# Performance work log

Hardware: AMD Instinct MI355X
Metric: run time of the kernel (lower is better)

The kernel has to match this reference:

```python
import jax, jax.numpy as jnp
import numpy as np

SPECIES = [1, 6, 7, 8]
N_SPECIES = len(SPECIES)
MAX_Z = max(SPECIES) + 1  # 9
N_IN = 256
N_HIDDEN = 512
N_OUT = 1
N_ATOMS = 65536


def setup_inputs() -> dict:
    key = jax.random.key(0)
    ks = jax.random.split(key, 9)
    x = jax.random.normal(ks[0], (N_ATOMS, N_IN), dtype=jnp.float32)
    z = jax.random.randint(ks[1], (N_ATOMS,), 0, MAX_Z)
    s = 0.05
    # Stacked per-species MLP parameters: [S, ...]
    W1 = jax.random.normal(ks[2], (N_SPECIES, N_HIDDEN, N_IN), dtype=jnp.float32) * s
    b1 = jax.random.normal(ks[3], (N_SPECIES, N_HIDDEN), dtype=jnp.float32) * s
    W2 = jax.random.normal(ks[4], (N_SPECIES, N_HIDDEN, N_HIDDEN), dtype=jnp.float32) * s
    b2 = jax.random.normal(ks[5], (N_SPECIES, N_HIDDEN), dtype=jnp.float32) * s
    W3 = jax.random.normal(ks[6], (N_SPECIES, N_OUT, N_HIDDEN), dtype=jnp.float32) * s
    b3 = jax.random.normal(ks[7], (N_SPECIES, N_OUT), dtype=jnp.float32) * s
    # One-hot embedding table [MAX_Z, N_SPECIES]: row Z has 1.0 at its species slot
    E = np.zeros((MAX_Z, N_SPECIES), dtype=np.float32)
    for idx, Z in enumerate(SPECIES):
        E[Z, idx] = 1.0
    E = jnp.asarray(E)
    return {"x": x, "z": z, "W1": W1, "b1": b1, "W2": W2, "b2": b2,
            "W3": W3, "b3": b3, "E": E}


def reference(x, z, W1, b1, W2, b2, W3, b3, E):
    # Every atom runs through all species MLPs (dense, O(N*S)), as in the original.
    # h1: [N, S, H]
    h1 = jnp.tanh(jnp.einsum('ni,shi->nsh', x, W1) + b1[None])
    h2 = jnp.tanh(jnp.einsum('nsh,sgh->nsg', h1, W2) + b2[None])
    # out_s: [N, S, n_out] -> [N, S*n_out] (n_out == 1 -> [N, S])
    out_s = (jnp.einsum('nsh,soh->nso', h2, W3) + b3[None]).reshape(x.shape[0], -1)
    gate = E[z]  # [N, S] embedding lookup (one-hot hard routing)
    return jnp.sum(out_s * gate, axis=1)  # [N]
```

## Files before the change

kernel.cpp:

```cpp
#include <hip/hip_runtime.h>

typedef __attribute__((ext_vector_type(8))) short bf16x8;
typedef __attribute__((ext_vector_type(4))) float f32x4;
typedef __attribute__((ext_vector_type(2))) unsigned int u32x2;
typedef unsigned short us;

#define NATOMS 65536
#define NIN 256
#define NHID 512
#define TM 128
#define LDB 528

__device__ __forceinline__ us f2b(float f) {
    union { float f; unsigned int u; } a; a.f = f;
    unsigned int r = a.u + 0x7FFFu + ((a.u >> 16) & 1u);
    return (us)(r >> 16);
}
__device__ __forceinline__ float fast_tanh(float v) {
    float t = __builtin_amdgcn_exp2f(v * 2.88539008f);
    float r = __builtin_amdgcn_rcpf(t + 1.f);
    return __builtin_fmaf(-2.f, r, 1.f);
}
__device__ __forceinline__ unsigned cvt_pk(float lo, float hi) {
    unsigned p;
    asm("v_cvt_pk_bf16_f32 %0, %1, %2" : "=v"(p) : "v"(lo), "v"(hi));
    return p;
}

__global__ __launch_bounds__(1024) void setup_kernel(
    const float* __restrict__ W1, const float* __restrict__ W2,
    const float* __restrict__ W3,
    us* __restrict__ W1p, us* __restrict__ W2p, us* __restrict__ W3b,
    const int* __restrict__ z, int* __restrict__ cnt,
    int* __restrict__ lists, float* __restrict__ out) {
    int tid = threadIdx.x;
    int blk = blockIdx.x;
    if (blk < 64) {
        __shared__ int lcnt[4];
        __shared__ int gbase[4];
        __shared__ int wbase[16][4];
        int wv = tid >> 6;
        int lane = tid & 63;
        if (tid < 4) lcnt[tid] = 0;
        __syncthreads();

        int i = blk * 1024 + tid;
        int zz = z[i];
        int s = (zz == 1) ? 0 : (zz == 6) ? 1 : (zz == 7) ? 2 : (zz == 8) ? 3 : -1;
        if (s < 0) out[i] = 0.f;

        int prefix = 0;
#pragma unroll
        for (int sp = 0; sp < 4; ++sp) {
            unsigned long long m = __ballot(s == sp);
            if (m) {
                int c = __popcll(m);
                int leader = __ffsll((long long)m) - 1;
                if (lane == leader) wbase[wv][sp] = atomicAdd(&lcnt[sp], c);
                if (s == sp) prefix = __popcll(m & ((1ull << lane) - 1ull));
            }
        }
        __syncthreads();
        if (tid < 4) gbase[tid] = atomicAdd(&cnt[tid], lcnt[tid]);
        __syncthreads();
        if (s >= 0) lists[s * NATOMS + gbase[s] + wbase[wv][s] + prefix] = i;
    } else {
        int i = (blk - 64) * 1024 + tid;
        if (i < 65536) {
            int s = i >> 14;
            int n = (i >> 5) & 511;
            int k8 = i & 31;
            const float* src = W1 + (size_t)i * 8;
            us p[8];
#pragma unroll
            for (int j = 0; j < 8; ++j) p[j] = f2b(src[j]);
            int ntile = n >> 4, nl = n & 15;
            int kstep = k8 >> 2, kq = k8 & 3;
            int lane = kq * 16 + nl;
            size_t chunk = ((size_t)(s * 32 + ntile) * 8 + kstep) * 64 + lane;
            *(uint4*)(W1p + chunk * 8) = *(uint4*)p;
        }
        if (i < 131072) {
            int s = i >> 15;
            int n = (i >> 6) & 511;
            int k8 = i & 63;
            const float* src = W2 + (size_t)i * 8;
            us p[8];
#pragma unroll
            for (int j = 0; j < 8; ++j) p[j] = f2b(src[j]);
            int ntile = n >> 4, nl = n & 15;
            int kstep = k8 >> 2, kq = k8 & 3;
            int lane = kq * 16 + nl;
            size_t chunk = ((size_t)(s * 32 + ntile) * 16 + kstep) * 64 + lane;
            *(uint4*)(W2p + chunk * 8) = *(uint4*)p;
        }
        if (i < 2048) W3b[i] = f2b(W3[i]);
    }
}

template<int K>
__device__ __forceinline__ void gemm8(const char* ldsLo, const char* ldsHi, const us* Wp,
                                      int lane, int wtile, f32x4 acc[8][4]) {
    constexpr int KS = K / 32;
    const us* wp[4];
#pragma unroll
    for (int nt = 0; nt < 4; ++nt)
        wp[nt] = Wp + (((size_t)(wtile + nt) * KS) * 64 + lane) * 8;
    int aoff[8];
#pragma unroll
    for (int mt = 0; mt < 8; ++mt)
        aoff[mt] = (mt * 16 + (lane & 15)) * LDB + (((lane >> 4) << 3) << 1);

    bf16x8 a0[4], a1[4], b[2][4];
#pragma unroll
    for (int nt = 0; nt < 4; ++nt) b[0][nt] = *(const bf16x8*)wp[nt];
#pragma unroll
    for (int mt = 0; mt < 4; ++mt) a0[mt] = *(const bf16x8*)(ldsLo + aoff[mt]);

#pragma unroll
    for (int i = 0; i < KS; ++i) {
        const int bc = i & 1;
        const char* srcI = (i < 8) ? (ldsLo + i * 64) : (ldsHi + (i - 8) * 64);
#pragma unroll
        for (int mt = 0; mt < 4; ++mt)
            a1[mt] = *(const bf16x8*)(srcI + aoff[4 + mt]);
        if (i + 1 < KS) {
#pragma unroll
            for (int nt = 0; nt < 4; ++nt)
                b[bc ^ 1][nt] = *(const bf16x8*)(wp[nt] + (i + 1) * 512);
        }
        __builtin_amdgcn_s_setprio(1);
#pragma unroll
        for (int nt = 0; nt < 4; ++nt)
#pragma unroll
            for (int mt = 0; mt < 4; ++mt)
                acc[mt][nt] = __builtin_amdgcn_mfma_f32_16x16x32_bf16(a0[mt], b[bc][nt], acc[mt][nt], 0, 0, 0);
        __builtin_amdgcn_s_setprio(0);
        if (i + 1 < KS) {
            const char* srcN = (i + 1 < 8) ? (ldsLo + (i + 1) * 64) : (ldsHi + (i + 1 - 8) * 64);
#pragma unroll
            for (int mt = 0; mt < 4; ++mt)
                a0[mt] = *(const bf16x8*)(srcN + aoff[mt]);
        }
        __builtin_amdgcn_s_setprio(1);
#pragma unroll
        for (int nt = 0; nt < 4; ++nt)
#pragma unroll
            for (int mt = 0; mt < 4; ++mt)
                acc[4 + mt][nt] = __builtin_amdgcn_mfma_f32_16x16x32_bf16(a1[mt], b[bc][nt], acc[4 + mt][nt], 0, 0, 0);
        __builtin_amdgcn_s_setprio(0);
    }
}

__device__ __forceinline__ void act_store_split(char* bufA, char* bufB,
                                                const float* __restrict__ bias,
                                                int lane, int ncb, f32x4 acc[8][4]) {
    char* dstBase = (ncb < 256) ? bufA : bufB;
    int coff = (ncb < 256) ? ncb : (ncb - 256);
#pragma unroll
    for (int nt = 0; nt < 4; ++nt) {
        int nl = coff + nt * 16 + (lane & 15);
        float bv = bias[ncb + nt * 16 + (lane & 15)];
#pragma unroll
        for (int mt = 0; mt < 8; ++mt) {
            float t0 = fast_tanh(acc[mt][nt][0] + bv);
            float t1 = fast_tanh(acc[mt][nt][1] + bv);
            float t2 = fast_tanh(acc[mt][nt][2] + bv);
            float t3 = fast_tanh(acc[mt][nt][3] + bv);
            unsigned p01 = cvt_pk(t0, t1);
            unsigned p23 = cvt_pk(t2, t3);
            int row0 = mt * 16 + ((lane >> 4) << 2);
            char* base = dstBase + row0 * LDB + nl * 2;
            *(us*)(base)           = (us)p01;
            *(us*)(base + LDB)     = (us)(p01 >> 16);
            *(us*)(base + 2 * LDB) = (us)p23;
            *(us*)(base + 3 * LDB) = (us)(p23 >> 16);
        }
    }
}

__global__ __launch_bounds__(512, 1) void mlp_kernel(
    const float* __restrict__ x, const int* __restrict__ cnt, const int* __restrict__ lists,
    const us* __restrict__ W1p, const us* __restrict__ W2p, const us* __restrict__ W3b,
    const float* __restrict__ b1, const float* __restrict__ b2, const float* __restrict__ b3,
    float* __restrict__ out) {
    int bx = blockIdx.x;
    int s = bx & 3;
    int t = bx >> 2;
    int base = t * TM;
    int n_s = cnt[s];
    if (base >= n_s) return;
    const int* list = lists + s * NATOMS;
    int cnt_t = n_s - base; if (cnt_t > TM) cnt_t = TM;

    __shared__ __align__(16) char bufA[TM * LDB];
    __shared__ __align__(16) char bufB[TM * LDB];

    int tid = threadIdx.x;
    int lane = tid & 63;
    int w = tid >> 6;
    int wtile = w * 4;
    int ncb = w * 64;

    {
        int r = tid >> 2;
        int cb = (tid & 3) * 64;
        int atom = (r < cnt_t) ? list[base + r] : -1;
        const float* xr = x + (size_t)(atom < 0 ? 0 : atom) * NIN;
#pragma unroll
        for (int j = 0; j < 16; ++j) {
            int c = cb + j * 4;
            float4 v;
            if (atom >= 0) v = *(const float4*)(xr + c);
            else v = make_float4(0.f, 0.f, 0.f, 0.f);
            u32x2 p;
            p.x = cvt_pk(v.x, v.y);
            p.y = cvt_pk(v.z, v.w);
            *(u32x2*)(bufB + r * LDB + c * 2) = p;
        }
    }
    __syncthreads();

    {
        f32x4 acc[8][4];
#pragma unroll
        for (int i = 0; i < 8; ++i)
#pragma unroll
            for (int j = 0; j < 4; ++j) acc[i][j] = (f32x4){0.f, 0.f, 0.f, 0.f};
        gemm8<NIN>(bufB, bufB, W1p + (size_t)s * NHID * NIN, lane, wtile, acc);
        __syncthreads();
        act_store_split(bufA, bufB, b1 + s * NHID, lane, ncb, acc);
    }
    __syncthreads();

    {
        f32x4 acc[8][4];
#pragma unroll
        for (int i = 0; i < 8; ++i)
#pragma unroll
            for (int j = 0; j < 4; ++j) acc[i][j] = (f32x4){0.f, 0.f, 0.f, 0.f};
        gemm8<NHID>(bufA, bufB, W2p + (size_t)s * NHID * NHID, lane, wtile, acc);
        __syncthreads();
        act_store_split(bufA, bufB, b2 + s * NHID, lane, ncb, acc);
    }
    __syncthreads();

    {
        int m = tid >> 2;
        int q = tid & 3;
        const us* W3s = W3b + (size_t)s * NHID;
        const char* src = (q < 2) ? bufA : bufB;
        int cbase = (q < 2) ? q * 128 : q * 128 - 256;
        float sum = 0.f;
#pragma unroll
        for (int j = 0; j < 16; ++j) {
            int hh = cbase + j * 8;
            bf16x8 hv = *(const bf16x8*)(src + m * LDB + hh * 2);
            bf16x8 wv = *(const bf16x8*)(W3s + q * 128 + j * 8);
#pragma unroll
            for (int e = 0; e < 8; ++e) {
                union { unsigned u; float f; } ha, wa;
                ha.u = ((unsigned)(us)hv[e]) << 16;
                wa.u = ((unsigned)(us)wv[e]) << 16;
                sum += ha.f * wa.f;
            }
        }
        sum += __shfl_xor(sum, 1);
        sum += __shfl_xor(sum, 2);
        if (q == 0 && m < cnt_t) out[list[base + m]] = sum + b3[s];
    }
}

extern "C" void kernel_launch(void* const* d_in, const int* in_sizes, int n_in,
                              void* d_out, int out_size, void* d_ws, size_t ws_size,
                              hipStream_t stream) {
    const float* x  = (const float*)d_in[0];
    const int*   z  = (const int*)d_in[1];
    const float* W1 = (const float*)d_in[2];
    const float* b1 = (const float*)d_in[3];
    const float* W2 = (const float*)d_in[4];
    const float* b2 = (const float*)d_in[5];
    const float* W3 = (const float*)d_in[6];
    const float* b3 = (const float*)d_in[7];
    float* out = (float*)d_out;

    char* ws = (char*)d_ws;
    int* cnt = (int*)ws;
    int* lists = (int*)(ws + 256);
    us* W1p = (us*)(ws + 256 + (size_t)4 * NATOMS * 4);
    us* W2p = W1p + 4 * NHID * NIN;
    us* W3b = W2p + 4 * NHID * NHID;

    (void)hipMemsetAsync(cnt, 0, 16, stream);
    setup_kernel<<<192, 1024, 0, stream>>>(W1, W2, W3, W1p, W2p, W3b, z, cnt, lists, out);
    mlp_kernel<<<256, 512, 0, stream>>>(x, cnt, lists, W1p, W2p, W3b, b1, b2, b3, out);
}
```

Baseline: 55.29 us.

## Split fused MLP into layer1 and layer2+3 kernels with smaller tiles

Replaces the single fused 128-row MLP kernel with two kernels: layer 1 writes bf16 hidden activations to a workspace buffer, then layer 2+3 reads them back in 32-row tiles. The smaller tiles give more blocks (512 and 1024 instead of 256) to fill the GPU's compute units and shrink per-block LDS. The cost is an extra launch plus a global round trip of the h1 activations. The fused path is kept as a fallback when the workspace is too small, and the per-species MAXROWS cap of 8192 assumes each species gets at most that many atoms.

```diff
diff --git a/kernel.cpp b/kernel.cpp
--- a/kernel.cpp
+++ b/kernel.cpp
@@ -10,6 +10,9 @@
 #define NHID 512
 #define TM 128
 #define LDB 528
+#define MAXROWS 8192
+#define LDBX 528
+#define LDBH 1040
 
 __device__ __forceinline__ us f2b(float f) {
     union { float f; unsigned int u; } a; a.f = f;
@@ -271,6 +274,231 @@
     }
 }
 
+__global__ __launch_bounds__(512, 1) void layer1_kernel(
+    const float* __restrict__ x, const int* __restrict__ cnt, const int* __restrict__ lists,
+    const us* __restrict__ W1p, const float* __restrict__ b1, us* __restrict__ h1buf) {
+    int bx = blockIdx.x;
+    int s = bx & 3;
+    int t = bx >> 2;
+    int base = t * 64;
+    int n_s = cnt[s];
+    if (base >= n_s) return;
+    const int* list = lists + s * NATOMS;
+    int cnt_t = n_s - base; if (cnt_t > 64) cnt_t = 64;
+
+    __shared__ __align__(16) char bufX[64 * LDBX];
+
+    int tid = threadIdx.x;
+    int lane = tid & 63;
+    int w = tid >> 6;
+    int wtile = w * 4;
+    int ncb = w * 64;
+
+    {
+        int r = tid >> 3;
+        int cb = (tid & 7) * 32;
+        int atom = (r < cnt_t) ? list[base + r] : -1;
+        const float* xr = x + (size_t)(atom < 0 ? 0 : atom) * NIN;
+#pragma unroll
+        for (int j = 0; j < 8; ++j) {
+            int c = cb + j * 4;
+            float4 v;
+            if (atom >= 0) v = *(const float4*)(xr + c);
+            else v = make_float4(0.f, 0.f, 0.f, 0.f);
+            u32x2 p;
+            p.x = cvt_pk(v.x, v.y);
+            p.y = cvt_pk(v.z, v.w);
+            *(u32x2*)(bufX + r * LDBX + c * 2) = p;
+        }
+    }
+    __syncthreads();
+
+    f32x4 acc[4][4];
+#pragma unroll
+    for (int i = 0; i < 4; ++i)
+#pragma unroll
+        for (int j = 0; j < 4; ++j) acc[i][j] = (f32x4){0.f, 0.f, 0.f, 0.f};
+    {
+        const us* Wp = W1p + (size_t)s * NHID * NIN;
+        const us* wp[4];
+#pragma unroll
+        for (int nt = 0; nt < 4; ++nt)
+            wp[nt] = Wp + (((size_t)(wtile + nt) * 8) * 64 + lane) * 8;
+        int aoff[4];
+#pragma unroll
+        for (int mt = 0; mt < 4; ++mt)
+            aoff[mt] = (mt * 16 + (lane & 15)) * LDBX + (((lane >> 4) << 3) << 1);
+
+        bf16x8 b[2][4];
+#pragma unroll
+        for (int nt = 0; nt < 4; ++nt) b[0][nt] = *(const bf16x8*)wp[nt];
+#pragma unroll
+        for (int i = 0; i < 8; ++i) {
+            const int bc = i & 1;
+            if (i + 1 < 8) {
+#pragma unroll
+                for (int nt = 0; nt < 4; ++nt)
+                    b[bc ^ 1][nt] = *(const bf16x8*)(wp[nt] + (i + 1) * 512);
+            }
+            bf16x8 a[4];
+#pragma unroll
+            for (int mt = 0; mt < 4; ++mt)
+                a[mt] = *(const bf16x8*)(bufX + aoff[mt] + i * 64);
+            __builtin_amdgcn_s_setprio(1);
+#pragma unroll
+            for (int nt = 0; nt < 4; ++nt)
+#pragma unroll
+                for (int mt = 0; mt < 4; ++mt)
+                    acc[mt][nt] = __builtin_amdgcn_mfma_f32_16x16x32_bf16(b[bc][nt], a[mt], acc[mt][nt], 0, 0, 0);
+            __builtin_amdgcn_s_setprio(0);
+        }
+    }
+
+    us* h1seg = h1buf + (size_t)s * MAXROWS * NHID;
+#pragma unroll
+    for (int nt = 0; nt < 4; ++nt) {
+        int n0 = ncb + nt * 16 + ((lane >> 4) << 2);
+        float4 bv = *(const float4*)(b1 + s * NHID + n0);
+#pragma unroll
+        for (int mt = 0; mt < 4; ++mt) {
+            int m = mt * 16 + (lane & 15);
+            float t0 = fast_tanh(acc[mt][nt][0] + bv.x);
+            float t1 = fast_tanh(acc[mt][nt][1] + bv.y);
+            float t2 = fast_tanh(acc[mt][nt][2] + bv.z);
+            float t3 = fast_tanh(acc[mt][nt][3] + bv.w);
+            u32x2 p;
+            p.x = cvt_pk(t0, t1);
+            p.y = cvt_pk(t2, t3);
+            if (m < cnt_t)
+                *(u32x2*)(h1seg + (size_t)(base + m) * NHID + n0) = p;
+        }
+    }
+}
+
+__global__ __launch_bounds__(512, 1) void layer23_kernel(
+    const int* __restrict__ cnt, const int* __restrict__ lists,
+    const us* __restrict__ h1buf, const us* __restrict__ W2p, const us* __restrict__ W3b,
+    const float* __restrict__ b2, const float* __restrict__ b3,
+    float* __restrict__ out) {
+    int bx = blockIdx.x;
+    int s = bx & 3;
+    int t = bx >> 2;
+    int base = t * 32;
+    int n_s = cnt[s];
+    if (base >= n_s) return;
+    const int* list = lists + s * NATOMS;
+    int cnt_t = n_s - base; if (cnt_t > 32) cnt_t = 32;
+
+    __shared__ __align__(16) char bufH[32 * LDBH];
+
+    int tid = threadIdx.x;
+    int lane = tid & 63;
+    int w = tid >> 6;
+    int wtile = w * 4;
+    int ncb = w * 64;
+
+    const us* h1seg = h1buf + (size_t)s * MAXROWS * NHID;
+
+    {
+        int r = tid >> 4;
+        int cq = tid & 15;
+        int rr = (r < cnt_t) ? r : (cnt_t - 1);
+        const us* src = h1seg + (size_t)(base + rr) * NHID + cq * 32;
+        char* dst = bufH + r * LDBH + cq * 64;
+        *(uint4*)(dst)      = *(const uint4*)(src);
+        *(uint4*)(dst + 16) = *(const uint4*)(src + 8);
+        *(uint4*)(dst + 32) = *(const uint4*)(src + 16);
+        *(uint4*)(dst + 48) = *(const uint4*)(src + 24);
+    }
+    __syncthreads();
+
+    f32x4 acc[2][4];
+#pragma unroll
+    for (int i = 0; i < 2; ++i)
+#pragma unroll
+        for (int j = 0; j < 4; ++j) acc[i][j] = (f32x4){0.f, 0.f, 0.f, 0.f};
+    {
+        const us* Wp = W2p + (size_t)s * NHID * NHID;
+        const us* wp[4];
+#pragma unroll
+        for (int nt = 0; nt < 4; ++nt)
+            wp[nt] = Wp + (((size_t)(wtile + nt) * 16) * 64 + lane) * 8;
+        int aoff[2];
+#pragma unroll
+        for (int mt = 0; mt < 2; ++mt)
+            aoff[mt] = (mt * 16 + (lane & 15)) * LDBH + (((lane >> 4) << 3) << 1);
+
+        bf16x8 b[2][4];
+#pragma unroll
+        for (int nt = 0; nt < 4; ++nt) b[0][nt] = *(const bf16x8*)wp[nt];
+#pragma unroll
+        for (int i = 0; i < 16; ++i) {
+            const int bc = i & 1;
+            if (i + 1 < 16) {
+#pragma unroll
+                for (int nt = 0; nt < 4; ++nt)
+                    b[bc ^ 1][nt] = *(const bf16x8*)(wp[nt] + (i + 1) * 512);
+            }
+            bf16x8 a[2];
+#pragma unroll
+            for (int mt = 0; mt < 2; ++mt)
+                a[mt] = *(const bf16x8*)(bufH + aoff[mt] + i * 64);
+            __builtin_amdgcn_s_setprio(1);
+#pragma unroll
+            for (int nt = 0; nt < 4; ++nt)
+#pragma unroll
+                for (int mt = 0; mt < 2; ++mt)
+                    acc[mt][nt] = __builtin_amdgcn_mfma_f32_16x16x32_bf16(b[bc][nt], a[mt], acc[mt][nt], 0, 0, 0);
+            __builtin_amdgcn_s_setprio(0);
+        }
+    }
+    __syncthreads();
+
+#pragma unroll
+    for (int nt = 0; nt < 4; ++nt) {
+        int n0 = ncb + nt * 16 + ((lane >> 4) << 2);
+        float4 bv = *(const float4*)(b2 + s * NHID + n0);
+#pragma unroll
+        for (int mt = 0; mt < 2; ++mt) {
+            int m = mt * 16 + (lane & 15);
+            float t0 = fast_tanh(acc[mt][nt][0] + bv.x);
+            float t1 = fast_tanh(acc[mt][nt][1] + bv.y);
+            float t2 = fast_tanh(acc[mt][nt][2] + bv.z);
+            float t3 = fast_tanh(acc[mt][nt][3] + bv.w);
+            u32x2 p;
+            p.x = cvt_pk(t0, t1);
+            p.y = cvt_pk(t2, t3);
+            *(u32x2*)(bufH + m * LDBH + n0 * 2) = p;
+        }
+    }
+    __syncthreads();
+
+    {
+        int m = tid >> 4;
+        int q = tid & 15;
+        const us* W3s = W3b + (size_t)s * NHID;
+        float sum = 0.f;
+#pragma unroll
+        for (int j = 0; j < 4; ++j) {
+            int hh = q * 32 + j * 8;
+            bf16x8 hv = *(const bf16x8*)(bufH + m * LDBH + hh * 2);
+            bf16x8 wv = *(const bf16x8*)(W3s + hh);
+#pragma unroll
+            for (int e = 0; e < 8; ++e) {
+                union { unsigned u; float f; } ha, wa;
+                ha.u = ((unsigned)(us)hv[e]) << 16;
+                wa.u = ((unsigned)(us)wv[e]) << 16;
+                sum += ha.f * wa.f;
+            }
+        }
+        sum += __shfl_xor(sum, 1);
+        sum += __shfl_xor(sum, 2);
+        sum += __shfl_xor(sum, 4);
+        sum += __shfl_xor(sum, 8);
+        if (q == 0 && m < cnt_t) out[list[base + m]] = sum + b3[s];
+    }
+}
+
 extern "C" void kernel_launch(void* const* d_in, const int* in_sizes, int n_in,
                               void* d_out, int out_size, void* d_ws, size_t ws_size,
                               hipStream_t stream) {
@@ -290,8 +518,21 @@
     us* W1p = (us*)(ws + 256 + (size_t)4 * NATOMS * 4);
     us* W2p = W1p + 4 * NHID * NIN;
     us* W3b = W2p + 4 * NHID * NHID;
+    us* h1buf = W3b + 4 * NHID;
+
+    const size_t NEEDED_SPLIT = 256
+        + (size_t)4 * NATOMS * 4
+        + (size_t)4 * NHID * NIN * 2
+        + (size_t)4 * NHID * NHID * 2
+        + (size_t)4 * NHID * 2
+        + (size_t)4 * MAXROWS * NHID * 2;
 
     (void)hipMemsetAsync(cnt, 0, 16, stream);
     setup_kernel<<<192, 1024, 0, stream>>>(W1, W2, W3, W1p, W2p, W3b, z, cnt, lists, out);
-    mlp_kernel<<<256, 512, 0, stream>>>(x, cnt, lists, W1p, W2p, W3b, b1, b2, b3, out);
-}
+    if (ws_size >= NEEDED_SPLIT) {
+        layer1_kernel<<<512, 512, 0, stream>>>(x, cnt, lists, W1p, b1, h1buf);
+        layer23_kernel<<<1024, 512, 0, stream>>>(cnt, lists, h1buf, W2p, W3b, b2, b3, out);
+    } else {
+        mlp_kernel<<<256, 512, 0, stream>>>(x, cnt, lists, W1p, W2p, W3b, b1, b2, b3, out);
+    }
+}
```

Result: slower. 71.77 us (+29.8%).
